# Kernel tuning notes

Hardware: AMD Instinct MI355X
Metric: run time of the kernel (lower is better)

Reference implementation:

```python
import jax, jax.numpy as jnp
import numpy as np


def setup_inputs() -> dict:
    key = jax.random.key(0)
    k1, k2 = jax.random.split(key)
    B, Tq, Tk, D = 8, 2048, 2048, 1024
    decoder_hidden = jax.random.normal(k1, (B, Tq, D), dtype=jnp.float32)
    encoder_outputs = jax.random.normal(k2, (B, Tk, D), dtype=jnp.float32)
    return {"decoder_hidden": decoder_hidden, "encoder_outputs": encoder_outputs}


def reference(decoder_hidden, encoder_outputs):
    # scores: [B, Tq, Tk] = decoder_hidden @ encoder_outputs^T (no scaling, as in source)
    scores = jnp.einsum("bqd,bkd->bqk", decoder_hidden, encoder_outputs)
    attention_weights = jax.nn.softmax(scores, axis=2)
    # context: [B, Tq, D]
    context_vector = jnp.einsum("bqk,bkd->bqd", attention_weights, encoder_outputs)
    return (context_vector, attention_weights)
```

## Files before the change

### kernel.cpp

```cpp
#include <hip/hip_runtime.h>


typedef _Float16 f16;
typedef _Float16 half4 __attribute__((ext_vector_type(4)));
typedef _Float16 half8 __attribute__((ext_vector_type(8)));
typedef float floatx16 __attribute__((ext_vector_type(16)));

__device__ __forceinline__ void gl2lds16(const void* g, void* l) {
    __builtin_amdgcn_global_load_lds(
        (const __attribute__((address_space(1))) unsigned int*)g,
        (__attribute__((address_space(3))) unsigned int*)l,
        16, 0, 0);
}

__device__ __forceinline__ unsigned lds_off(const void* p) {
    return (unsigned)(unsigned long long)
        (const __attribute__((address_space(3))) void*)p;
}

__device__ __forceinline__ half8 dsr(unsigned a) {
    half8 r;
    asm volatile("ds_read_b128 %0, %1" : "=v"(r) : "v"(a));
    return r;
}

#define MFMA(a, b, c) __builtin_amdgcn_mfma_f32_32x32x16_f16((a), (b), (c), 0, 0, 0)
#define WAIT_LGKM0() asm volatile("s_waitcnt lgkmcnt(0)" ::: "memory")
#define WAIT_LGKM8() asm volatile("s_waitcnt lgkmcnt(8)" ::: "memory")
#define WAIT_VM6()   asm volatile("s_waitcnt vmcnt(6)" ::: "memory")
#define WAIT_VM0()   asm volatile("s_waitcnt vmcnt(0)" ::: "memory")
#define SBAR()       __builtin_amdgcn_s_barrier()
#define SCHED0()     __builtin_amdgcn_sched_barrier(0)

__global__ __launch_bounds__(256) void cvt_f32_f16(const float* __restrict__ src,
                                                   f16* __restrict__ dst, int n4) {
    int i = blockIdx.x * 256 + threadIdx.x;
    if (i >= n4) return;
    float4 v = ((const float4*)src)[i];
    half4 h;
    h[0] = (f16)v.x; h[1] = (f16)v.y; h[2] = (f16)v.z; h[3] = (f16)v.w;
    ((half4*)dst)[i] = h;
}

__global__ __launch_bounds__(256) void k_cvt_transpose(const float* __restrict__ K,
                                                       f16* __restrict__ Kh,
                                                       f16* __restrict__ Kt) {
    __shared__ f16 tile[64][72];
    const int b  = blockIdx.z;
    const int k0 = blockIdx.y * 64;
    const int d0 = blockIdx.x * 64;
    const float* src = K + (size_t)b * 2048 * 1024;
    f16* khb = Kh + (size_t)b * 2048 * 1024;
    f16* ktb = Kt + (size_t)b * 1024 * 2048;
    const int r  = threadIdx.x >> 4;
    const int c4 = (threadIdx.x & 15) * 4;
    #pragma unroll
    for (int it = 0; it < 4; it++) {
        int kr = it * 16 + r;
        float4 v = *(const float4*)&src[(size_t)(k0 + kr) * 1024 + d0 + c4];
        half4 h;
        h[0] = (f16)v.x; h[1] = (f16)v.y; h[2] = (f16)v.z; h[3] = (f16)v.w;
        *(half4*)&khb[(size_t)(k0 + kr) * 1024 + d0 + c4] = h;
        *(half4*)&tile[kr][c4] = h;
    }
    __syncthreads();
    #pragma unroll
    for (int it = 0; it < 4; it++) {
        int dr = it * 16 + r;
        half4 h;
        h[0] = tile[c4 + 0][dr]; h[1] = tile[c4 + 1][dr];
        h[2] = tile[c4 + 2][dr]; h[3] = tile[c4 + 3][dr];
        *(half4*)&ktb[(size_t)(d0 + dr) * 2048 + k0 + c4] = h;
    }
}

__global__ __launch_bounds__(512, 2) void gemm_bt8(const f16* __restrict__ Amat,
                                                   const f16* __restrict__ Bmat,
                                                   float* __restrict__ C,
                                                   int K_, int N, int nN,
                                                   long sA, long sB, long sC) {
    __shared__ __align__(16) f16 LA[2][2][8192];
    __shared__ __align__(16) f16 LB[2][2][8192];
    const int tid  = threadIdx.x;
    const int lane = tid & 63;
    const int wave = tid >> 6;
    const int wm   = wave >> 2;
    const int wn   = wave & 3;
    const int bz   = blockIdx.x;
    const int tileM = (blockIdx.y / nN) * 256;
    const int tileN = (blockIdx.y % nN) * 256;
    const f16* Ab = Amat + (size_t)bz * sA;
    const f16* Bb = Bmat + (size_t)bz * sB;
    float* Cb = C + (size_t)bz * sC;
    const int NT = K_ >> 6;
    const size_t g2 = (size_t)128 * K_;

    const int r0  = tid >> 3;
    const int gcc = (tid & 7) ^ (r0 & 7);
    const f16* sAp = Ab + (size_t)(tileM + r0) * K_ + gcc * 8;
    const f16* sBp = Bb + (size_t)(tileN + (r0 & 31) + (r0 >> 5) * 64) * K_ + gcc * 8;

    const int r31 = lane & 31;
    const int kh  = lane >> 5;
    const int sw  = lane & 7;
    const unsigned baseA0 = lds_off(&LA[0][0][0]) + (unsigned)((r31 + (wm << 6)) * 128);
    const unsigned baseB0 = lds_off(&LB[0][0][0]) + (unsigned)(((wn << 5) + r31) * 128);
    const unsigned pc0 = (unsigned)(((0 + kh) ^ sw) << 4);
    const unsigned pc1 = (unsigned)(((2 + kh) ^ sw) << 4);
    const unsigned pc2 = (unsigned)(((4 + kh) ^ sw) << 4);
    const unsigned pc3 = (unsigned)(((6 + kh) ^ sw) << 4);

    floatx16 acc00 = {0.f}, acc01 = {0.f}, acc10 = {0.f}, acc11 = {0.f};
    floatx16 acc20 = {0.f}, acc21 = {0.f}, acc30 = {0.f}, acc31 = {0.f};
    #pragma unroll
    for (int r = 0; r < 16; r++) {
        acc00[r] = 0.f; acc01[r] = 0.f; acc10[r] = 0.f; acc11[r] = 0.f;
        acc20[r] = 0.f; acc21[r] = 0.f; acc30[r] = 0.f; acc31[r] = 0.f;
    }

#define STAGE_A(P, H, SRC) do { const f16* _s = (SRC); f16* _d = &LA[P][H][tid * 8]; \
        gl2lds16(_s, _d); gl2lds16(_s + g2, _d + 4096); } while (0)
#define STAGE_B(P, H, SRC) do { const f16* _s = (SRC); f16* _d = &LB[P][H][tid * 8]; \
        gl2lds16(_s, _d); gl2lds16(_s + g2, _d + 4096); } while (0)

    STAGE_A(0, 0, sAp);
    STAGE_B(0, 0, sBp);
    STAGE_A(0, 1, sAp + (size_t)64 * K_);
    STAGE_B(0, 1, sBp + (size_t)32 * K_);
    STAGE_A(1, 0, sAp + 64);
    STAGE_B(1, 0, sBp + 64);
    STAGE_A(1, 1, sAp + (size_t)64 * K_ + 64);
    WAIT_VM6();
    SBAR();

    const f16* gB1 = sBp + (size_t)32 * K_ + 64;
    const f16* gA0 = sAp + 128;
    const f16* gB0 = sBp + 128;
    const f16* gA1 = sAp + (size_t)64 * K_ + 128;

    for (int T = 0; T < NT; ++T) {
        const int par = T & 1;
        const unsigned bA = baseA0 + (unsigned)(par << 15);
        const unsigned bB = baseB0 + (unsigned)(par << 15);

        half8 a00 = dsr(bA + pc0),        a01 = dsr(bA + pc1);
        half8 a02 = dsr(bA + pc2),        a03 = dsr(bA + pc3);
        half8 a10 = dsr(bA + 4096 + pc0), a11 = dsr(bA + 4096 + pc1);
        half8 a12 = dsr(bA + 4096 + pc2), a13 = dsr(bA + 4096 + pc3);
        half8 b00 = dsr(bB + pc0),        b01 = dsr(bB + pc1);
        half8 b02 = dsr(bB + pc2),        b03 = dsr(bB + pc3);
        if (T + 1 < NT) STAGE_B(par ^ 1, 1, gB1);
        WAIT_LGKM8();
        SBAR();
        WAIT_LGKM0();
        SCHED0();
        __builtin_amdgcn_s_setprio(1);
        acc00 = MFMA(a00, b00, acc00); acc10 = MFMA(a10, b00, acc10);
        acc00 = MFMA(a01, b01, acc00); acc10 = MFMA(a11, b01, acc10);
        acc00 = MFMA(a02, b02, acc00); acc10 = MFMA(a12, b02, acc10);
        acc00 = MFMA(a03, b03, acc00); acc10 = MFMA(a13, b03, acc10);
        __builtin_amdgcn_s_setprio(0);
        SCHED0();
        SBAR();
        half8 b10 = dsr(bB + 16384 + pc0), b11 = dsr(bB + 16384 + pc1);
        half8 b12 = dsr(bB + 16384 + pc2), b13 = dsr(bB + 16384 + pc3);
        if (T + 2 < NT) STAGE_A(par, 0, gA0);
        SBAR();
        WAIT_LGKM0();
        SCHED0();
        __builtin_amdgcn_s_setprio(1);
        acc01 = MFMA(a00, b10, acc01); acc11 = MFMA(a10, b10, acc11);
        acc01 = MFMA(a01, b11, acc01); acc11 = MFMA(a11, b11, acc11);
        acc01 = MFMA(a02, b12, acc01); acc11 = MFMA(a12, b12, acc11);
        acc01 = MFMA(a03, b13, acc01); acc11 = MFMA(a13, b13, acc11);
        __builtin_amdgcn_s_setprio(0);
        SCHED0();
        SBAR();
        half8 a20 = dsr(bA + 16384 + pc0),        a21 = dsr(bA + 16384 + pc1);
        half8 a22 = dsr(bA + 16384 + pc2),        a23 = dsr(bA + 16384 + pc3);
        half8 a30 = dsr(bA + 20480 + pc0),        a31 = dsr(bA + 20480 + pc1);
        half8 a32 = dsr(bA + 20480 + pc2),        a33 = dsr(bA + 20480 + pc3);
        if (T + 2 < NT) STAGE_B(par, 0, gB0);
        SBAR();
        WAIT_LGKM0();
        SCHED0();
        __builtin_amdgcn_s_setprio(1);
        acc21 = MFMA(a20, b10, acc21); acc31 = MFMA(a30, b10, acc31);
        acc21 = MFMA(a21, b11, acc21); acc31 = MFMA(a31, b11, acc31);
        acc21 = MFMA(a22, b12, acc21); acc31 = MFMA(a32, b12, acc31);
        acc21 = MFMA(a23, b13, acc21); acc31 = MFMA(a33, b13, acc31);
        __builtin_amdgcn_s_setprio(0);
        SCHED0();
        SBAR();
        if (T + 2 < NT) {
            STAGE_A(par, 1, gA1);
            WAIT_VM6();
        } else {
            WAIT_VM0();
        }
        SBAR();
        SCHED0();
        __builtin_amdgcn_s_setprio(1);
        acc20 = MFMA(a20, b00, acc20); acc30 = MFMA(a30, b00, acc30);
        acc20 = MFMA(a21, b01, acc20); acc30 = MFMA(a31, b01, acc30);
        acc20 = MFMA(a22, b02, acc20); acc30 = MFMA(a32, b02, acc30);
        acc20 = MFMA(a23, b03, acc20); acc30 = MFMA(a33, b03, acc30);
        __builtin_amdgcn_s_setprio(0);
        SCHED0();
        SBAR();
        gB1 += 64; gA0 += 64; gB0 += 64; gA1 += 64;
    }

#define EPI(ACC, F, G) do { \
        int col   = tileN + (wn << 6) + ((G) << 5) + r31; \
        int rbase = tileM + (wm << 7) + ((F) << 5) + (kh << 2); \
        _Pragma("unroll") \
        for (int r = 0; r < 16; r++) { \
            int row = rbase + (r & 3) + ((r >> 2) << 3); \
            Cb[(size_t)row * N + col] = ACC[r]; \
        } } while (0)
    EPI(acc00, 0, 0); EPI(acc01, 0, 1);
    EPI(acc10, 1, 0); EPI(acc11, 1, 1);
    EPI(acc20, 2, 0); EPI(acc21, 2, 1);
    EPI(acc30, 3, 0); EPI(acc31, 3, 1);
#undef EPI
#undef STAGE_A
#undef STAGE_B
}

__global__ __launch_bounds__(256) void softmax_rows(float* __restrict__ S,
                                                    f16* __restrict__ Wh) {
    const size_t row = blockIdx.x;
    float* p = S + row * 2048;
    f16* ph = Wh + row * 2048;
    const int tid = threadIdx.x;
    const int lane = tid & 63;
    const int wave = tid >> 6;
    __shared__ float red[8];

    float4 va = ((const float4*)p)[tid];
    float4 vb = ((const float4*)p)[tid + 256];
    float m = fmaxf(fmaxf(fmaxf(va.x, va.y), fmaxf(va.z, va.w)),
                    fmaxf(fmaxf(vb.x, vb.y), fmaxf(vb.z, vb.w)));
    #pragma unroll
    for (int off = 32; off; off >>= 1) m = fmaxf(m, __shfl_xor(m, off));
    if (lane == 0) red[wave] = m;
    __syncthreads();
    m = fmaxf(fmaxf(red[0], red[1]), fmaxf(red[2], red[3]));

    va.x = __expf(va.x - m); va.y = __expf(va.y - m);
    va.z = __expf(va.z - m); va.w = __expf(va.w - m);
    vb.x = __expf(vb.x - m); vb.y = __expf(vb.y - m);
    vb.z = __expf(vb.z - m); vb.w = __expf(vb.w - m);
    float s = va.x + va.y + va.z + va.w + vb.x + vb.y + vb.z + vb.w;
    #pragma unroll
    for (int off = 32; off; off >>= 1) s += __shfl_xor(s, off);
    if (lane == 0) red[4 + wave] = s;
    __syncthreads();
    s = red[4] + red[5] + red[6] + red[7];
    float inv = 1.0f / s;
    va.x *= inv; va.y *= inv; va.z *= inv; va.w *= inv;
    vb.x *= inv; vb.y *= inv; vb.z *= inv; vb.w *= inv;
    ((float4*)p)[tid] = va;
    ((float4*)p)[tid + 256] = vb;
    half4 ha, hb;
    ha[0] = (f16)va.x; ha[1] = (f16)va.y; ha[2] = (f16)va.z; ha[3] = (f16)va.w;
    hb[0] = (f16)vb.x; hb[1] = (f16)vb.y; hb[2] = (f16)vb.z; hb[3] = (f16)vb.w;
    ((half4*)ph)[tid] = ha;
    ((half4*)ph)[tid + 256] = hb;
}

extern "C" void kernel_launch(void* const* d_in, const int* in_sizes, int n_in,
                              void* d_out, int out_size, void* d_ws, size_t ws_size,
                              hipStream_t stream) {
    const float* Q = (const float*)d_in[0];
    const float* K = (const float*)d_in[1];
    float* ctx = (float*)d_out;
    float* W   = (float*)d_out + 16777216;

    f16* Qh = (f16*)d_ws;
    f16* Kh = Qh + 16777216;
    f16* Kt = Kh + 16777216;
    f16* Wh = (f16*)d_ws;

    cvt_f32_f16<<<16384, 256, 0, stream>>>(Q, Qh, 4194304);
    k_cvt_transpose<<<dim3(16, 32, 8), 256, 0, stream>>>(K, Kh, Kt);

    gemm_bt8<<<dim3(8, 64), 512, 0, stream>>>(
        Qh, Kh, W, 1024, 2048, 8, 2048L * 1024, 2048L * 1024, 2048L * 2048);

    softmax_rows<<<16384, 256, 0, stream>>>(W, Wh);

    gemm_bt8<<<dim3(8, 32), 512, 0, stream>>>(
        Wh, Kt, ctx, 2048, 1024, 4, 2048L * 2048, 1024L * 2048, 2048L * 1024);
}
```

Measured before the change: 472.8 us.

## Fuse conversion, both GEMMs and softmax into one cooperative persistent kernel

Replaces the five separate launches (Q conversion, K convert/transpose, scores GEMM, softmax, context GEMM) with a single cooperative kernel of 256 blocks that moves between phases via grid-wide syncs. The GEMM body becomes a device function that takes its shared-memory buffers as arguments. Softmax is rewritten so each wave owns whole rows, which removes the block-level reductions. This removes per-launch overhead and inter-kernel gaps. The cost is that the scores GEMM now runs its 512 tiles two at a time per block at lower concurrency, and each grid sync makes every block wait for the slowest one.

Result: slower. 625.8 us (+32.4%).

```diff
diff --git a/kernel.cpp b/kernel.cpp
--- a/kernel.cpp
+++ b/kernel.cpp
@@ -1,4 +1,7 @@
 #include <hip/hip_runtime.h>
+#include <hip/hip_cooperative_groups.h>
+
+namespace cg = cooperative_groups;
 
 
 typedef _Float16 f16;
@@ -32,67 +35,16 @@
 #define SBAR()       __builtin_amdgcn_s_barrier()
 #define SCHED0()     __builtin_amdgcn_sched_barrier(0)
 
-__global__ __launch_bounds__(256) void cvt_f32_f16(const float* __restrict__ src,
-                                                   f16* __restrict__ dst, int n4) {
-    int i = blockIdx.x * 256 + threadIdx.x;
-    if (i >= n4) return;
-    float4 v = ((const float4*)src)[i];
-    half4 h;
-    h[0] = (f16)v.x; h[1] = (f16)v.y; h[2] = (f16)v.z; h[3] = (f16)v.w;
-    ((half4*)dst)[i] = h;
-}
-
-__global__ __launch_bounds__(256) void k_cvt_transpose(const float* __restrict__ K,
-                                                       f16* __restrict__ Kh,
-                                                       f16* __restrict__ Kt) {
-    __shared__ f16 tile[64][72];
-    const int b  = blockIdx.z;
-    const int k0 = blockIdx.y * 64;
-    const int d0 = blockIdx.x * 64;
-    const float* src = K + (size_t)b * 2048 * 1024;
-    f16* khb = Kh + (size_t)b * 2048 * 1024;
-    f16* ktb = Kt + (size_t)b * 1024 * 2048;
-    const int r  = threadIdx.x >> 4;
-    const int c4 = (threadIdx.x & 15) * 4;
-    #pragma unroll
-    for (int it = 0; it < 4; it++) {
-        int kr = it * 16 + r;
-        float4 v = *(const float4*)&src[(size_t)(k0 + kr) * 1024 + d0 + c4];
-        half4 h;
-        h[0] = (f16)v.x; h[1] = (f16)v.y; h[2] = (f16)v.z; h[3] = (f16)v.w;
-        *(half4*)&khb[(size_t)(k0 + kr) * 1024 + d0 + c4] = h;
-        *(half4*)&tile[kr][c4] = h;
-    }
-    __syncthreads();
-    #pragma unroll
-    for (int it = 0; it < 4; it++) {
-        int dr = it * 16 + r;
-        half4 h;
-        h[0] = tile[c4 + 0][dr]; h[1] = tile[c4 + 1][dr];
-        h[2] = tile[c4 + 2][dr]; h[3] = tile[c4 + 3][dr];
-        *(half4*)&ktb[(size_t)(d0 + dr) * 2048 + k0 + c4] = h;
-    }
-}
-
-__global__ __launch_bounds__(512, 2) void gemm_bt8(const f16* __restrict__ Amat,
-                                                   const f16* __restrict__ Bmat,
-                                                   float* __restrict__ C,
-                                                   int K_, int N, int nN,
-                                                   long sA, long sB, long sC) {
-    __shared__ __align__(16) f16 LA[2][2][8192];
-    __shared__ __align__(16) f16 LB[2][2][8192];
-    const int tid  = threadIdx.x;
+__device__ __forceinline__ void gemm_tile(const f16* __restrict__ Ab,
+                                          const f16* __restrict__ Bb,
+                                          float* __restrict__ Cb,
+                                          int K_, int N, int tileM, int tileN,
+                                          f16* LAb, f16* LBb, int tid) {
     const int lane = tid & 63;
     const int wave = tid >> 6;
     const int wm   = wave >> 2;
     const int wn   = wave & 3;
-    const int bz   = blockIdx.x;
-    const int tileM = (blockIdx.y / nN) * 256;
-    const int tileN = (blockIdx.y % nN) * 256;
-    const f16* Ab = Amat + (size_t)bz * sA;
-    const f16* Bb = Bmat + (size_t)bz * sB;
-    float* Cb = C + (size_t)bz * sC;
-    const int NT = K_ >> 6;
+    const int NT   = K_ >> 6;
     const size_t g2 = (size_t)128 * K_;
 
     const int r0  = tid >> 3;
@@ -103,24 +55,25 @@
     const int r31 = lane & 31;
     const int kh  = lane >> 5;
     const int sw  = lane & 7;
-    const unsigned baseA0 = lds_off(&LA[0][0][0]) + (unsigned)((r31 + (wm << 6)) * 128);
-    const unsigned baseB0 = lds_off(&LB[0][0][0]) + (unsigned)(((wn << 5) + r31) * 128);
+    const unsigned baseA0 = lds_off(LAb) + (unsigned)((r31 + (wm << 6)) * 128);
+    const unsigned baseB0 = lds_off(LBb) + (unsigned)(((wn << 5) + r31) * 128);
     const unsigned pc0 = (unsigned)(((0 + kh) ^ sw) << 4);
     const unsigned pc1 = (unsigned)(((2 + kh) ^ sw) << 4);
     const unsigned pc2 = (unsigned)(((4 + kh) ^ sw) << 4);
     const unsigned pc3 = (unsigned)(((6 + kh) ^ sw) << 4);
 
-    floatx16 acc00 = {0.f}, acc01 = {0.f}, acc10 = {0.f}, acc11 = {0.f};
-    floatx16 acc20 = {0.f}, acc21 = {0.f}, acc30 = {0.f}, acc31 = {0.f};
+    floatx16 acc00, acc01, acc10, acc11, acc20, acc21, acc30, acc31;
     #pragma unroll
     for (int r = 0; r < 16; r++) {
         acc00[r] = 0.f; acc01[r] = 0.f; acc10[r] = 0.f; acc11[r] = 0.f;
         acc20[r] = 0.f; acc21[r] = 0.f; acc30[r] = 0.f; acc31[r] = 0.f;
     }
 
-#define STAGE_A(P, H, SRC) do { const f16* _s = (SRC); f16* _d = &LA[P][H][tid * 8]; \
+#define STAGE_A(P, H, SRC) do { const f16* _s = (SRC); \
+        f16* _d = LAb + (P) * 16384 + (H) * 8192 + tid * 8; \
         gl2lds16(_s, _d); gl2lds16(_s + g2, _d + 4096); } while (0)
-#define STAGE_B(P, H, SRC) do { const f16* _s = (SRC); f16* _d = &LB[P][H][tid * 8]; \
+#define STAGE_B(P, H, SRC) do { const f16* _s = (SRC); \
+        f16* _d = LBb + (P) * 16384 + (H) * 8192 + tid * 8; \
         gl2lds16(_s, _d); gl2lds16(_s + g2, _d + 4096); } while (0)
 
     STAGE_A(0, 0, sAp);
@@ -228,46 +181,142 @@
 #undef STAGE_B
 }
 
-__global__ __launch_bounds__(256) void softmax_rows(float* __restrict__ S,
-                                                    f16* __restrict__ Wh) {
-    const size_t row = blockIdx.x;
-    float* p = S + row * 2048;
-    f16* ph = Wh + row * 2048;
-    const int tid = threadIdx.x;
-    const int lane = tid & 63;
-    const int wave = tid >> 6;
-    __shared__ float red[8];
-
-    float4 va = ((const float4*)p)[tid];
-    float4 vb = ((const float4*)p)[tid + 256];
-    float m = fmaxf(fmaxf(fmaxf(va.x, va.y), fmaxf(va.z, va.w)),
-                    fmaxf(fmaxf(vb.x, vb.y), fmaxf(vb.z, vb.w)));
-    #pragma unroll
-    for (int off = 32; off; off >>= 1) m = fmaxf(m, __shfl_xor(m, off));
-    if (lane == 0) red[wave] = m;
-    __syncthreads();
-    m = fmaxf(fmaxf(red[0], red[1]), fmaxf(red[2], red[3]));
-
-    va.x = __expf(va.x - m); va.y = __expf(va.y - m);
-    va.z = __expf(va.z - m); va.w = __expf(va.w - m);
-    vb.x = __expf(vb.x - m); vb.y = __expf(vb.y - m);
-    vb.z = __expf(vb.z - m); vb.w = __expf(vb.w - m);
-    float s = va.x + va.y + va.z + va.w + vb.x + vb.y + vb.z + vb.w;
-    #pragma unroll
-    for (int off = 32; off; off >>= 1) s += __shfl_xor(s, off);
-    if (lane == 0) red[4 + wave] = s;
-    __syncthreads();
-    s = red[4] + red[5] + red[6] + red[7];
-    float inv = 1.0f / s;
-    va.x *= inv; va.y *= inv; va.z *= inv; va.w *= inv;
-    vb.x *= inv; vb.y *= inv; vb.z *= inv; vb.w *= inv;
-    ((float4*)p)[tid] = va;
-    ((float4*)p)[tid + 256] = vb;
-    half4 ha, hb;
-    ha[0] = (f16)va.x; ha[1] = (f16)va.y; ha[2] = (f16)va.z; ha[3] = (f16)va.w;
-    hb[0] = (f16)vb.x; hb[1] = (f16)vb.y; hb[2] = (f16)vb.z; hb[3] = (f16)vb.w;
-    ((half4*)ph)[tid] = ha;
-    ((half4*)ph)[tid + 256] = hb;
+__global__ __launch_bounds__(512, 2) void fused_attn(
+    const float* __restrict__ Q, const float* __restrict__ Kin,
+    float* __restrict__ ctx, float* __restrict__ W,
+    f16* __restrict__ Qh, f16* __restrict__ Kh,
+    f16* __restrict__ Kt, f16* __restrict__ Wh) {
+    __shared__ __align__(16) f16 LA[2][2][8192];
+    __shared__ __align__(16) f16 LB[2][2][8192];
+    const int tid   = threadIdx.x;
+    const int bid   = blockIdx.x;
+    const int batch = bid & 7;
+    const int bq    = bid >> 3;
+    cg::grid_group grid = cg::this_grid();
+
+    {
+        const float4* Q4 = (const float4*)Q;
+        half4* Qh4 = (half4*)Qh;
+        const int base = bid * 512 + tid;
+        for (int o = 0; o < 8; o++) {
+            float4 v[4];
+            #pragma unroll
+            for (int i = 0; i < 4; i++)
+                v[i] = Q4[(size_t)(o * 4 + i) * 131072 + base];
+            #pragma unroll
+            for (int i = 0; i < 4; i++) {
+                half4 h;
+                h[0] = (f16)v[i].x; h[1] = (f16)v[i].y;
+                h[2] = (f16)v[i].z; h[3] = (f16)v[i].w;
+                Qh4[(size_t)(o * 4 + i) * 131072 + base] = h;
+            }
+        }
+    }
+    {
+        f16* tile = &LA[0][0][0];
+        const float* src = Kin + (size_t)batch * 2048 * 1024;
+        f16* khb = Kh + (size_t)batch * 2048 * 1024;
+        f16* ktb = Kt + (size_t)batch * 1024 * 2048;
+        const int r  = tid >> 4;
+        const int c4 = (tid & 15) * 4;
+        for (int t = 0; t < 16; t++) {
+            const int idx = bq * 16 + t;
+            const int d0 = (idx & 15) * 64;
+            const int k0 = (idx >> 4) * 64;
+            __syncthreads();
+            #pragma unroll
+            for (int it = 0; it < 2; it++) {
+                int kr = it * 32 + r;
+                float4 v = *(const float4*)&src[(size_t)(k0 + kr) * 1024 + d0 + c4];
+                half4 h;
+                h[0] = (f16)v.x; h[1] = (f16)v.y; h[2] = (f16)v.z; h[3] = (f16)v.w;
+                *(half4*)&khb[(size_t)(k0 + kr) * 1024 + d0 + c4] = h;
+                *(half4*)&tile[kr * 72 + c4] = h;
+            }
+            __syncthreads();
+            #pragma unroll
+            for (int it = 0; it < 2; it++) {
+                int dr = it * 32 + r;
+                half4 h;
+                h[0] = tile[(c4 + 0) * 72 + dr]; h[1] = tile[(c4 + 1) * 72 + dr];
+                h[2] = tile[(c4 + 2) * 72 + dr]; h[3] = tile[(c4 + 3) * 72 + dr];
+                *(half4*)&ktb[(size_t)(d0 + dr) * 2048 + k0 + c4] = h;
+            }
+        }
+    }
+    grid.sync();
+
+    {
+        const f16* Ab = Qh + (size_t)batch * 2048 * 1024;
+        const f16* Bb = Kh + (size_t)batch * 2048 * 1024;
+        float* Cb = W + (size_t)batch * 2048 * 2048;
+        for (int rep = 0; rep < 2; rep++) {
+            const int y = bq + rep * 32;
+            gemm_tile(Ab, Bb, Cb, 1024, 2048, (y >> 3) * 256, (y & 7) * 256,
+                      &LA[0][0][0], &LB[0][0][0], tid);
+        }
+    }
+    grid.sync();
+
+    {
+        const int wave = tid >> 6, lane = tid & 63;
+        float* Sb = W + ((size_t)batch * 2048 + (size_t)bq * 64) * 2048;
+        f16* Whb  = Wh + ((size_t)batch * 2048 + (size_t)bq * 64) * 2048;
+        for (int jj = 0; jj < 2; jj++) {
+            float4 v[4][8];
+            #pragma unroll
+            for (int j = 0; j < 4; j++) {
+                const int row = wave * 8 + jj * 4 + j;
+                const float4* p = (const float4*)(Sb + (size_t)row * 2048);
+                #pragma unroll
+                for (int i = 0; i < 8; i++) v[j][i] = p[lane + i * 64];
+            }
+            #pragma unroll
+            for (int j = 0; j < 4; j++) {
+                const int row = wave * 8 + jj * 4 + j;
+                float m = -1e30f;
+                #pragma unroll
+                for (int i = 0; i < 8; i++)
+                    m = fmaxf(m, fmaxf(fmaxf(v[j][i].x, v[j][i].y),
+                                       fmaxf(v[j][i].z, v[j][i].w)));
+                #pragma unroll
+                for (int off = 32; off; off >>= 1) m = fmaxf(m, __shfl_xor(m, off));
+                float s = 0.f;
+                #pragma unroll
+                for (int i = 0; i < 8; i++) {
+                    v[j][i].x = __expf(v[j][i].x - m);
+                    v[j][i].y = __expf(v[j][i].y - m);
+                    v[j][i].z = __expf(v[j][i].z - m);
+                    v[j][i].w = __expf(v[j][i].w - m);
+                    s += v[j][i].x + v[j][i].y + v[j][i].z + v[j][i].w;
+                }
+                #pragma unroll
+                for (int off = 32; off; off >>= 1) s += __shfl_xor(s, off);
+                const float inv = 1.0f / s;
+                float4* pw = (float4*)(Sb + (size_t)row * 2048);
+                half4* ph = (half4*)(Whb + (size_t)row * 2048);
+                #pragma unroll
+                for (int i = 0; i < 8; i++) {
+                    v[j][i].x *= inv; v[j][i].y *= inv;
+                    v[j][i].z *= inv; v[j][i].w *= inv;
+                    pw[lane + i * 64] = v[j][i];
+                    half4 h;
+                    h[0] = (f16)v[j][i].x; h[1] = (f16)v[j][i].y;
+                    h[2] = (f16)v[j][i].z; h[3] = (f16)v[j][i].w;
+                    ph[lane + i * 64] = h;
+                }
+            }
+        }
+    }
+    grid.sync();
+
+    {
+        const f16* Ab = Wh + (size_t)batch * 2048 * 2048;
+        const f16* Bb = Kt + (size_t)batch * 1024 * 2048;
+        float* Cb = ctx + (size_t)batch * 2048 * 1024;
+        gemm_tile(Ab, Bb, Cb, 2048, 1024, (bq >> 2) * 256, (bq & 3) * 256,
+                  &LA[0][0][0], &LB[0][0][0], tid);
+    }
 }
 
 extern "C" void kernel_launch(void* const* d_in, const int* in_sizes, int n_in,
@@ -283,14 +332,8 @@
     f16* Kt = Kh + 16777216;
     f16* Wh = (f16*)d_ws;
 
-    cvt_f32_f16<<<16384, 256, 0, stream>>>(Q, Qh, 4194304);
-    k_cvt_transpose<<<dim3(16, 32, 8), 256, 0, stream>>>(K, Kh, Kt);
-
-    gemm_bt8<<<dim3(8, 64), 512, 0, stream>>>(
-        Qh, Kh, W, 1024, 2048, 8, 2048L * 1024, 2048L * 1024, 2048L * 2048);
-
-    softmax_rows<<<16384, 256, 0, stream>>>(W, Wh);
-
-    gemm_bt8<<<dim3(8, 32), 512, 0, stream>>>(
-        Wh, Kt, ctx, 2048, 1024, 4, 2048L * 2048, 1024L * 2048, 2048L * 1024);
-}
+    void* args[] = {(void*)&Q, (void*)&K, (void*)&ctx, (void*)&W,
+                    (void*)&Qh, (void*)&Kh, (void*)&Kt, (void*)&Wh};
+    hipLaunchCooperativeKernel((const void*)fused_attn, dim3(256), dim3(512),
+                               args, 0, stream);
+}
```
